# Kernel tuning notes

Hardware: AMD Instinct MI355X
Metric: run time of the kernel (lower is better)

Reference implementation:

```python
import jax, jax.numpy as jnp
from jax import lax
import numpy as np

B, S, G = 64, 200, 8
CHAR_V, GAZ_V = 8000, 100000
D_CHAR, D_GAZ, H = 128, 128, 512
N_LABEL = 20
N_TAG = N_LABEL + 2  # CRF adds START (N_TAG-2) and STOP (N_TAG-1)


def setup_inputs() -> dict:
    key = jax.random.key(0)
    ks = jax.random.split(key, 16)
    lengths = jax.random.randint(ks[0], (B,), S // 2, S + 1)
    pos = jnp.arange(S)[None, :]
    mask = pos < lengths[:, None]
    char_inputs = jax.random.randint(ks[1], (B, S), 0, CHAR_V)
    gaz_ids = jax.random.randint(ks[2], (B, S, G), 0, GAZ_V)
    cnt = jax.random.randint(ks[3], (B, S), 1, G + 1)
    gaz_mask = (jnp.arange(G)[None, None, :] < cnt[..., None]).astype(jnp.int32)
    rev_gaz_ids = jax.random.randint(ks[4], (B, S, G), 0, GAZ_V)
    rcnt = jax.random.randint(ks[5], (B, S), 1, G + 1)
    rev_gaz_mask = (jnp.arange(G)[None, None, :] < rcnt[..., None]).astype(jnp.int32)
    sc = 0.1
    D_in = D_CHAR + D_GAZ
    return dict(
        char_inputs=char_inputs, lengths=lengths, mask=mask,
        gaz_ids=gaz_ids, gaz_mask=gaz_mask,
        rev_gaz_ids=rev_gaz_ids, rev_gaz_mask=rev_gaz_mask,
        char_table=jax.random.normal(ks[6], (CHAR_V, D_CHAR)) * sc,
        gaz_table=jax.random.normal(ks[7], (GAZ_V, D_GAZ)) * sc,
        w_ih_f=jax.random.normal(ks[8], (4 * H, D_in)) * sc,
        w_hh_f=jax.random.normal(ks[9], (4 * H, H)) * sc,
        b_f=jnp.zeros((4 * H,), jnp.float32),
        w_ih_b=jax.random.normal(ks[10], (4 * H, D_in)) * sc,
        w_hh_b=jax.random.normal(ks[11], (4 * H, H)) * sc,
        b_b=jnp.zeros((4 * H,), jnp.float32),
        W_out=jax.random.normal(ks[12], (2 * H, N_TAG)) * sc,
        b_out=jnp.zeros((N_TAG,), jnp.float32),
        transitions=jax.random.normal(ks[13], (N_TAG, N_TAG)) * sc,
    )


def rev_pad(x, lengths):
    # reverse each sequence within its valid length (reverse_padded_sequence)
    b, s = x.shape[0], x.shape[1]
    pos = jnp.arange(s)[None, :]
    idx = jnp.where(pos < lengths[:, None], lengths[:, None] - 1 - pos, pos)
    idx = idx.reshape((b, s) + (1,) * (x.ndim - 2))
    return jnp.take_along_axis(x, jnp.broadcast_to(idx, x.shape), axis=1)


def gaz_embed(table, ids, m):
    # masked mean over the G candidate gaz words per char (Gaz_Embed, type=1)
    e = table[ids]                                   # [B,S,G,D]
    mf = m.astype(e.dtype)[..., None]
    return (e * mf).sum(2) / jnp.maximum(mf.sum(2), 1.0)


def lstm(x, w_ih, w_hh, b):
    # x: [B,S,D]; torch gate order i,f,g,o
    h0 = jnp.zeros((x.shape[0], H), x.dtype)

    def step(carry, xt):
        h, c = carry
        g = xt @ w_ih.T + h @ w_hh.T + b
        i, f, gg, o = jnp.split(g, 4, axis=-1)
        c = jax.nn.sigmoid(f) * c + jax.nn.sigmoid(i) * jnp.tanh(gg)
        h = jax.nn.sigmoid(o) * jnp.tanh(c)
        return (h, c), h

    _, hs = lax.scan(step, (h0, h0), x.transpose(1, 0, 2))
    return hs.transpose(1, 0, 2)                     # [B,S,H]


def emissions_fn(char_inputs, lengths, gaz_ids, gaz_mask, rev_gaz_ids, rev_gaz_mask,
                 char_table, gaz_table, w_ih_f, w_hh_f, b_f, w_ih_b, w_hh_b, b_b,
                 W_out, b_out):
    char_embs = char_table[char_inputs]              # [B,S,Dc]
    rev_char_embs = rev_pad(char_embs, lengths)
    g_f = gaz_embed(gaz_table, gaz_ids, gaz_mask)
    g_b = gaz_embed(gaz_table, rev_pad(rev_gaz_ids, lengths), rev_pad(rev_gaz_mask, lengths))
    fwd_in = jnp.concatenate([char_embs, g_f], axis=-1)
    bwd_in = jnp.concatenate([rev_char_embs, g_b], axis=-1)
    h_f = lstm(fwd_in, w_ih_f, w_hh_f, b_f)
    h_b = rev_pad(lstm(bwd_in, w_ih_b, w_hh_b, b_b), lengths)
    lstm_outs = jnp.concatenate([h_f, h_b], axis=-1)  # [B,S,2H]
    return lstm_outs @ W_out + b_out                  # [B,S,N_TAG]


def viterbi(emissions, mask, transitions):
    # transitions[prev, next]; START=N_TAG-2, STOP=N_TAG-1
    n = emissions.shape[-1]
    start, stop = n - 2, n - 1
    init = emissions[:, 0] + transitions[start][None, :]     # [B,n]
    ident = jnp.arange(n, dtype=jnp.int32)[None, :]

    def vstep(part, inp):
        emit_t, m_t = inp                                    # [B,n], [B]
        cand = part[:, :, None] + transitions[None] + emit_t[:, None, :]
        new = cand.max(axis=1)
        bp = cand.argmax(axis=1).astype(jnp.int32)
        part = jnp.where(m_t[:, None], new, part)
        bp = jnp.where(m_t[:, None], bp, ident)              # identity bp on pad
        return part, bp

    part, bps = lax.scan(vstep, init,
                         (emissions[:, 1:].transpose(1, 0, 2), mask[:, 1:].T))
    last_tag = (part + transitions[:, stop][None, :]).argmax(-1).astype(jnp.int32)

    def btstep(tag, bp):
        prev = jnp.take_along_axis(bp, tag[:, None], axis=1)[:, 0]
        return prev, prev

    _, prev_tags = lax.scan(btstep, last_tag, bps, reverse=True)  # [S-1,B]
    tags = jnp.concatenate([prev_tags.T, last_tag[:, None]], axis=1)
    return tags * mask.astype(tags.dtype)


def reference(char_inputs, lengths, mask, gaz_ids, gaz_mask, rev_gaz_ids, rev_gaz_mask,
              char_table, gaz_table, w_ih_f, w_hh_f, b_f, w_ih_b, w_hh_b, b_b,
              W_out, b_out, transitions):
    emissions = emissions_fn(char_inputs, lengths, gaz_ids, gaz_mask,
                             rev_gaz_ids, rev_gaz_mask, char_table, gaz_table,
                             w_ih_f, w_hh_f, b_f, w_ih_b, w_hh_b, b_b, W_out, b_out)
    return viterbi(emissions, mask, transitions)
```

## Files before the change

### kernel.cpp

```cpp
#include <hip/hip_runtime.h>
#include <math.h>

#define S_LEN 200
#define BATCH 64
#define HID   512
#define NTAG  22
#define TCH   25
#define MC    (TCH*BATCH)

typedef unsigned short u16;
typedef unsigned int   u32;

__device__ __forceinline__ float bf2f(u16 u){
  union { u32 ui; float f; } v; v.ui = ((u32)u) << 16; return v.f;
}

__global__ void k_detect(const u32* __restrict__ w, int* __restrict__ flag){
  __shared__ int cnt;
  if (threadIdx.x == 0) cnt = 0;
  __syncthreads();
  int hits = 0;
  for (int i = threadIdx.x; i < 16384; i += 256){
    u32 e = (w[i] & 0x7F80u);
    if (e >= 0x3800u && e <= 0x4080u) hits++;
  }
  atomicAdd(&cnt, hits);
  __syncthreads();
  if (threadIdx.x == 0) *flag = (cnt > 8192) ? 1 : 0;
}

__global__ void k_cvt_f(const void* __restrict__ src, float* __restrict__ dst,
                        int n, const int* __restrict__ flag){
  int i = blockIdx.x*blockDim.x + threadIdx.x;
  if (i >= n) return;
  if (*flag) dst[i] = bf2f(((const u16*)src)[i]);
  else       dst[i] = ((const float*)src)[i];
}

__global__ void k_cvt4(const void* s0, float* d0, int n0,
                       const void* s1, float* d1, int n1,
                       const void* s2, float* d2, int n2,
                       const void* s3, float* d3, int n3,
                       const int* __restrict__ flag){
  int i = blockIdx.x*blockDim.x + threadIdx.x;
  int isbf = *flag;
  if (i < n0) d0[i] = isbf ? bf2f(((const u16*)s0)[i]) : ((const float*)s0)[i];
  if (i < n1) d1[i] = isbf ? bf2f(((const u16*)s1)[i]) : ((const float*)s1)[i];
  if (i < n2) d2[i] = isbf ? bf2f(((const u16*)s2)[i]) : ((const float*)s2)[i];
  if (i < n3) d3[i] = isbf ? bf2f(((const u16*)s3)[i]) : ((const float*)s3)[i];
}

__global__ __launch_bounds__(256)
void k_cvt_whh(const void* __restrict__ wf, const void* __restrict__ wb,
               float* __restrict__ dst, const int* __restrict__ flag){
  int o = blockIdx.x*256 + threadIdx.x;
  if (o >= 2*2048*512) return;
  int j = o & 63, r = (o>>6)&15, w = (o>>10)&7, slice = (o>>13)&127, dir = o>>20;
  int row = (r>>2)*512 + slice*4 + (r&3);
  int si = row*512 + w*64 + j;
  const void* src = dir ? wb : wf;
  float v = (*flag) ? bf2f(((const u16*)src)[si]) : ((const float*)src)[si];
  dst[o] = v;
}

__global__ void k_cvt_wt(const void* __restrict__ src, float* __restrict__ dst,
                         const int* __restrict__ flag){
  int i = blockIdx.x*blockDim.x + threadIdx.x;
  if (i >= 1024*24) return;
  int k = i / 24, tag = i % 24;
  float v = 0.f;
  if (tag < NTAG){
    v = (*flag) ? bf2f(((const u16*)src)[k*NTAG + tag])
                : ((const float*)src)[k*NTAG + tag];
  }
  int half = k >> 9, kk = k & 511;
  dst[((size_t)half*512 + kk)*24 + tag] = v;
}

__global__ void k_zero(float* __restrict__ p, int n){
  int i = blockIdx.x*blockDim.x + threadIdx.x;
  if (i < n) p[i] = 0.f;
}

__global__ __launch_bounds__(128)
void k_build(const int* __restrict__ ci, const int* __restrict__ lengths,
             const int* __restrict__ gid, const int* __restrict__ gm,
             const int* __restrict__ rgid, const int* __restrict__ rgm,
             const void* __restrict__ ctab, const void* __restrict__ gtab,
             const int* __restrict__ flag,
             float* __restrict__ fin, float* __restrict__ bin)
{
  int bs = blockIdx.x;
  int b = bs / S_LEN, s = bs % S_LEN;
  int d = threadIdx.x;
  int isbf = *flag;
  int len = lengths[b];
  int sb = (s < len) ? (len - 1 - s) : s;
  size_t orow = ((size_t)s*BATCH + b)*256;

  {
    int cid = ci[bs];
    float cv = isbf ? bf2f(((const u16*)ctab)[(size_t)cid*128 + d])
                    : ((const float*)ctab)[(size_t)cid*128 + d];
    fin[orow + d] = cv;
    const int* gg = gid + (size_t)bs*8;
    const int* mm = gm  + (size_t)bs*8;
    float sum = 0.f, cntf = 0.f;
    for (int g = 0; g < 8; ++g){
      float m = (float)mm[g];
      int gw = gg[g];
      float gv = isbf ? bf2f(((const u16*)gtab)[(size_t)gw*128 + d])
                      : ((const float*)gtab)[(size_t)gw*128 + d];
      sum += m * gv; cntf += m;
    }
    fin[orow + 128 + d] = sum / fmaxf(cntf, 1.f);
  }
  {
    int bsr = b*S_LEN + sb;
    int cid = ci[bsr];
    float cv = isbf ? bf2f(((const u16*)ctab)[(size_t)cid*128 + d])
                    : ((const float*)ctab)[(size_t)cid*128 + d];
    bin[orow + d] = cv;
    const int* gg = rgid + (size_t)bsr*8;
    const int* mm = rgm  + (size_t)bsr*8;
    float sum = 0.f, cntf = 0.f;
    for (int g = 0; g < 8; ++g){
      float m = (float)mm[g];
      int gw = gg[g];
      float gv = isbf ? bf2f(((const u16*)gtab)[(size_t)gw*128 + d])
                      : ((const float*)gtab)[(size_t)gw*128 + d];
      sum += m * gv; cntf += m;
    }
    bin[orow + 128 + d] = sum / fmaxf(cntf, 1.f);
  }
}

__global__ __launch_bounds__(256)
void k_gemm_ih(const float* __restrict__ Af, const float* __restrict__ Ab,
               const float* __restrict__ wih,
               const float* __restrict__ bias,
               float* __restrict__ gxc,
               int t0)
{
  const int dir = blockIdx.z;
  const float* A = (dir ? Ab : Af) + (size_t)t0*BATCH*256;
  const float* W = wih + (size_t)dir*2048*256;
  const float* bi = bias + (size_t)dir*2048;
  float* C = gxc + (size_t)dir*2048*MC;
  const int m0 = blockIdx.y * 64;
  const int n0 = blockIdx.x * 128;
  const int tid = threadIdx.x;
  __shared__ float As[32][64];
  __shared__ float Ws[32][128];
  const int lrA = tid >> 2, kqA = (tid & 3)*8;
  const int lrW = tid >> 1, kqW = (tid & 1)*16;
  const int tx = tid & 31, ty = tid >> 5;
  float acc[8][4] = {};

  for (int k0 = 0; k0 < 256; k0 += 32){
    float4 a0 = *(const float4*)(A + (size_t)(m0+lrA)*256 + k0+kqA);
    float4 a1 = *(const float4*)(A + (size_t)(m0+lrA)*256 + k0+kqA+4);
    float4 w0 = *(const float4*)(W + (size_t)(n0+lrW)*256 + k0+kqW);
    float4 w1 = *(const float4*)(W + (size_t)(n0+lrW)*256 + k0+kqW+4);
    float4 w2 = *(const float4*)(W + (size_t)(n0+lrW)*256 + k0+kqW+8);
    float4 w3 = *(const float4*)(W + (size_t)(n0+lrW)*256 + k0+kqW+12);
    As[kqA+0][lrA]=a0.x; As[kqA+1][lrA]=a0.y; As[kqA+2][lrA]=a0.z; As[kqA+3][lrA]=a0.w;
    As[kqA+4][lrA]=a1.x; As[kqA+5][lrA]=a1.y; As[kqA+6][lrA]=a1.z; As[kqA+7][lrA]=a1.w;
    Ws[kqW+ 0][lrW]=w0.x; Ws[kqW+ 1][lrW]=w0.y; Ws[kqW+ 2][lrW]=w0.z; Ws[kqW+ 3][lrW]=w0.w;
    Ws[kqW+ 4][lrW]=w1.x; Ws[kqW+ 5][lrW]=w1.y; Ws[kqW+ 6][lrW]=w1.z; Ws[kqW+ 7][lrW]=w1.w;
    Ws[kqW+ 8][lrW]=w2.x; Ws[kqW+ 9][lrW]=w2.y; Ws[kqW+10][lrW]=w2.z; Ws[kqW+11][lrW]=w2.w;
    Ws[kqW+12][lrW]=w3.x; Ws[kqW+13][lrW]=w3.y; Ws[kqW+14][lrW]=w3.z; Ws[kqW+15][lrW]=w3.w;
    __syncthreads();
    #pragma unroll 8
    for (int kk = 0; kk < 32; ++kk){
      float4 av0 = *(const float4*)(&As[kk][ty*8]);
      float4 av1 = *(const float4*)(&As[kk][ty*8+4]);
      float4 wv  = *(const float4*)(&Ws[kk][tx*4]);
      acc[0][0]+=av0.x*wv.x; acc[0][1]+=av0.x*wv.y; acc[0][2]+=av0.x*wv.z; acc[0][3]+=av0.x*wv.w;
      acc[1][0]+=av0.y*wv.x; acc[1][1]+=av0.y*wv.y; acc[1][2]+=av0.y*wv.z; acc[1][3]+=av0.y*wv.w;
      acc[2][0]+=av0.z*wv.x; acc[2][1]+=av0.z*wv.y; acc[2][2]+=av0.z*wv.z; acc[2][3]+=av0.z*wv.w;
      acc[3][0]+=av0.w*wv.x; acc[3][1]+=av0.w*wv.y; acc[3][2]+=av0.w*wv.z; acc[3][3]+=av0.w*wv.w;
      acc[4][0]+=av1.x*wv.x; acc[4][1]+=av1.x*wv.y; acc[4][2]+=av1.x*wv.z; acc[4][3]+=av1.x*wv.w;
      acc[5][0]+=av1.y*wv.x; acc[5][1]+=av1.y*wv.y; acc[5][2]+=av1.y*wv.z; acc[5][3]+=av1.y*wv.w;
      acc[6][0]+=av1.z*wv.x; acc[6][1]+=av1.z*wv.y; acc[6][2]+=av1.z*wv.z; acc[6][3]+=av1.z*wv.w;
      acc[7][0]+=av1.w*wv.x; acc[7][1]+=av1.w*wv.y; acc[7][2]+=av1.w*wv.z; acc[7][3]+=av1.w*wv.w;
    }
    __syncthreads();
  }

  #pragma unroll
  for (int jn = 0; jn < 4; ++jn){
    int col = n0 + tx*4 + jn;
    float bj = bi[col];
    float4 o0 = make_float4(acc[0][jn]+bj, acc[1][jn]+bj, acc[2][jn]+bj, acc[3][jn]+bj);
    float4 o1 = make_float4(acc[4][jn]+bj, acc[5][jn]+bj, acc[6][jn]+bj, acc[7][jn]+bj);
    *(float4*)(C + (size_t)col*MC + m0 + ty*8)     = o0;
    *(float4*)(C + (size_t)col*MC + m0 + ty*8 + 4) = o1;
  }
}

__global__ __launch_bounds__(512)
void k_step(const float* __restrict__ wsw,
            const float* __restrict__ gxc,
            float* __restrict__ hbuf,
            float* __restrict__ cbuf,
            float* __restrict__ hseq,
            int t, int tc)
{
  const int dir = blockIdx.y;
  const int slice = blockIdx.x;
  const int hrow_base = slice*4;
  const int tid = threadIdx.x;
  const int b = tid & 63;
  const int uw = __builtin_amdgcn_readfirstlane(tid >> 6);
  const int uk0 = uw * 64;

  __shared__ float part[8*16*64];

  const float* hprev = hbuf + (size_t)(dir*2 + (t&1))*HID*BATCH;
  float* hnext       = hbuf + (size_t)(dir*2 + ((t+1)&1))*HID*BATCH;

  float pgi=0.f, pgf=0.f, pgg=0.f, pgo=0.f, pc=0.f;
  if (tid < 256){
    const int hr = tid >> 6, bb = tid & 63;
    const int hrow = hrow_base + hr;
    const float* gxb = gxc + (size_t)dir*2048*MC + (size_t)tc*BATCH + bb;
    pgi = gxb[(size_t)(   0 + hrow)*MC];
    pgf = gxb[(size_t)( 512 + hrow)*MC];
    pgg = gxb[(size_t)(1024 + hrow)*MC];
    pgo = gxb[(size_t)(1536 + hrow)*MC];
    pc  = cbuf[((size_t)dir*HID + hrow)*BATCH + bb];
  }

  float hv[64];
  #pragma unroll
  for (int j = 0; j < 64; ++j)
    hv[j] = hprev[(size_t)(uk0 + j)*BATCH + b];

  const float* wv_base = wsw + (((size_t)(dir*128 + slice))*8 + uw)*1024;

  float acc[16];
  #pragma unroll
  for (int r = 0; r < 16; ++r) acc[r] = 0.f;

  #pragma unroll
  for (int r = 0; r < 16; ++r){
    const float* wr = wv_base + r*64;
    #pragma unroll
    for (int j = 0; j < 64; ++j)
      acc[r] += wr[j] * hv[j];
  }

  #pragma unroll
  for (int r = 0; r < 16; ++r)
    part[(uw*16 + r)*64 + b] = acc[r];
  __syncthreads();

  if (tid < 256){
    const int hr = tid >> 6;
    const int bb = tid & 63;
    const int hrow = hrow_base + hr;
    float g4[4];
    #pragma unroll
    for (int g = 0; g < 4; ++g){
      const int r = g*4 + hr;
      float s = 0.f;
      #pragma unroll
      for (int ww = 0; ww < 8; ++ww)
        s += part[(ww*16 + r)*64 + bb];
      g4[g] = s;
    }
    float gi = g4[0] + pgi;
    float gf = g4[1] + pgf;
    float gg = g4[2] + pgg;
    float go = g4[3] + pgo;
    float si = 1.f/(1.f+expf(-gi));
    float sf = 1.f/(1.f+expf(-gf));
    float so = 1.f/(1.f+expf(-go));
    float c = sf*pc + si*tanhf(gg);
    float h = so*tanhf(c);
    cbuf[((size_t)dir*HID + hrow)*BATCH + bb] = c;
    hnext[(size_t)hrow*BATCH + bb] = h;
    hseq[(((size_t)dir*S_LEN + t)*HID + hrow)*BATCH + bb] = h;
  }
}

__global__ __launch_bounds__(256)
void k_emis(const float* __restrict__ hseq, const int* __restrict__ lengths,
            const float* __restrict__ wpad,
            const float* __restrict__ bout,
            float* __restrict__ emisF, float* __restrict__ emisB)
{
  const int t = blockIdx.x;
  const int dir = blockIdx.y;
  const int tid = threadIdx.x;
  const int b = tid & 63;
  const int utg = __builtin_amdgcn_readfirstlane(tid >> 6);

  __shared__ float hl[64*64];

  const float* hsrc = hseq + ((size_t)(dir*S_LEN + t)*HID)*BATCH;
  const float* wbase = wpad + (size_t)dir*512*24 + utg*6;

  float acc[6] = {0.f,0.f,0.f,0.f,0.f,0.f};

  for (int c = 0; c < 8; ++c){
    const float4* s4 = (const float4*)(hsrc + (size_t)c*64*64);
    float4* d4 = (float4*)hl;
    #pragma unroll
    for (int q = 0; q < 4; ++q) d4[q*256 + tid] = s4[q*256 + tid];
    __syncthreads();
    const float* wrow = wbase + (size_t)c*64*24;
    #pragma unroll 4
    for (int k = 0; k < 64; ++k){
      float hval = hl[k*64 + b];
      #pragma unroll
      for (int i = 0; i < 6; ++i) acc[i] += hval * wrow[k*24 + i];
    }
    __syncthreads();
  }

  const int len = lengths[b];
  const int pos = dir ? ((t < len) ? (len - 1 - t) : t) : t;
  float* dst = (dir ? emisB : emisF) + ((size_t)b*S_LEN + pos)*NTAG;
  #pragma unroll
  for (int i = 0; i < 6; ++i){
    int tag = utg*6 + i;
    if (tag < NTAG) dst[tag] = acc[i] + (dir ? 0.f : bout[tag]);
  }
}

__global__ __launch_bounds__(64)
void k_viterbi(const float* __restrict__ emisF, const float* __restrict__ emisB,
               const int* __restrict__ lengths,
               const float* __restrict__ trans, int* __restrict__ out)
{
  const int b = blockIdx.x;
  const int j = threadIdx.x;
  __shared__ unsigned char bp[(S_LEN-1)*NTAG];
  const int len = lengths[b];
  const float* ef = emisF + (size_t)b*S_LEN*NTAG;
  const float* eb = emisB + (size_t)b*S_LEN*NTAG;
  const bool act = (j < NTAG);

  float trc[NTAG];
  #pragma unroll
  for (int i = 0; i < NTAG; ++i)
    trc[i] = act ? trans[i*NTAG + j] : 0.f;
  const float trstop = act ? trans[j*NTAG + (NTAG-1)] : 0.f;

  float part = act ? (ef[j] + eb[j] + trans[(NTAG-2)*NTAG + j]) : -3.4e38f;
  float e_next = act ? (ef[NTAG + j] + eb[NTAG + j]) : 0.f;

  for (int t = 1; t < S_LEN; ++t){
    float e = e_next;
    if (t+1 < S_LEN && act) e_next = ef[(t+1)*NTAG + j] + eb[(t+1)*NTAG + j];
    float best = -3.4e38f; int bi = 0;
    #pragma unroll
    for (int i = 0; i < NTAG; ++i){
      float v = __shfl(part, i) + trc[i];
      if (v > best){ best = v; bi = i; }
    }
    if (t < len) part = best + e;
    if (act) bp[(t-1)*NTAG + j] = (unsigned char)((t < len) ? bi : j);
  }

  float fin = part + trstop;
  float best = -3.4e38f; int tag = 0;
  #pragma unroll
  for (int i = 0; i < NTAG; ++i){
    float v = __shfl(fin, i);
    if (v > best){ best = v; tag = i; }
  }
  __builtin_amdgcn_wave_barrier();
  if (j == 0){
    out[b*S_LEN + S_LEN-1] = (S_LEN-1 < len) ? tag : 0;
    for (int t = S_LEN-2; t >= 0; --t){
      tag = bp[t*NTAG + tag];
      out[b*S_LEN + t] = (t < len) ? tag : 0;
    }
  }
}

extern "C" void kernel_launch(void* const* d_in, const int* in_sizes, int n_in,
                              void* d_out, int out_size, void* d_ws, size_t ws_size,
                              hipStream_t stream)
{
  (void)in_sizes; (void)n_in; (void)out_size; (void)ws_size;
  const int* char_inputs  = (const int*)d_in[0];
  const int* lengths      = (const int*)d_in[1];
  const int* gaz_ids      = (const int*)d_in[3];
  const int* gaz_mask     = (const int*)d_in[4];
  const int* rev_gaz_ids  = (const int*)d_in[5];
  const int* rev_gaz_mask = (const int*)d_in[6];
  const void* char_table  = d_in[7];
  const void* gaz_table   = d_in[8];
  const void* w_ih_f = d_in[9];
  const void* w_hh_f = d_in[10];
  const void* b_f    = d_in[11];
  const void* w_ih_b = d_in[12];
  const void* w_hh_b = d_in[13];
  const void* b_b    = d_in[14];
  const void* W_out  = d_in[15];
  const void* b_out  = d_in[16];
  const void* trans  = d_in[17];

  char* ws = (char*)d_ws;
  size_t off = 0;
  auto alloc = [&](size_t bytes)->char*{
    char* p = ws + off; off = (off + bytes + 255) & ~(size_t)255; return p;
  };
  int*   flag   = (int*)  alloc(256);
  float* wsw    = (float*)alloc(2ull*2048*512*4);
  float* wih32  = (float*)alloc(2ull*2048*256*4);
  float* bias32 = (float*)alloc(2ull*2048*4);
  float* wpad   = (float*)alloc(2ull*512*24*4);
  float* bout32 = (float*)alloc(22ull*4);
  float* trans32= (float*)alloc(484ull*4);
  float* fwd_in = (float*)alloc(12800ull*256*4);
  float* bwd_in = (float*)alloc(12800ull*256*4);
  float* gxc    = (float*)alloc(2ull*2048*MC*4);
  float* hbuf   = (float*)alloc(2ull*2*512*64*4);
  float* cbuf   = (float*)alloc(2ull*512*64*4);
  float* hseq   = (float*)alloc(2ull*200*512*64*4);
  float* emisF  = (float*)alloc(12800ull*22*4);
  float* emisB  = (float*)alloc(12800ull*22*4);

  k_detect<<<1,256,0,stream>>>((const u32*)char_table, flag);
  k_cvt_whh<<<8192,256,0,stream>>>(w_hh_f, w_hh_b, wsw, flag);
  k_cvt_f<<<2048,256,0,stream>>>(w_ih_f, wih32,          524288, flag);
  k_cvt_f<<<2048,256,0,stream>>>(w_ih_b, wih32 + 524288, 524288, flag);
  k_cvt4<<<8,256,0,stream>>>(b_f, bias32, 2048,
                             b_b, bias32 + 2048, 2048,
                             b_out, bout32, 22,
                             trans, trans32, 484, flag);
  k_cvt_wt<<<96,256,0,stream>>>(W_out, wpad, flag);

  k_build<<<12800,128,0,stream>>>(char_inputs, lengths, gaz_ids, gaz_mask,
                                  rev_gaz_ids, rev_gaz_mask, char_table, gaz_table,
                                  flag, fwd_in, bwd_in);

  k_zero<<<768,256,0,stream>>>(hbuf, 2*2*512*64 + 2*512*64);

  for (int t0 = 0; t0 < S_LEN; t0 += TCH){
    k_gemm_ih<<<dim3(16,TCH,2),256,0,stream>>>(fwd_in, bwd_in, wih32, bias32,
                                               gxc, t0);
    for (int tc = 0; tc < TCH; ++tc)
      k_step<<<dim3(128,2),512,0,stream>>>(wsw, gxc, hbuf, cbuf, hseq, t0+tc, tc);
  }

  k_emis<<<dim3(S_LEN,2),256,0,stream>>>(hseq, lengths, wpad, bout32, emisF, emisB);
  k_viterbi<<<64,64,0,stream>>>(emisF, emisB, lengths, trans32, (int*)d_out);
}
```

Baseline: 2.886 ms.

## Fuse per-timestep LSTM launches into cooperative kernel with grid sync

Replaces the 25 separate per-timestep LSTM step launches in each chunk with one cooperative kernel that loops over the timesteps and calls grid.sync between them. If the cooperative launch fails, it falls back to per-step launches. The aim is to remove kernel launch overhead and inter-launch gaps, at the cost of a grid-wide barrier per step. The Viterbi kernel also switches from wave shuffles to shared memory with block barriers, which adds two syncs per step.

```diff
diff --git a/kernel.cpp b/kernel.cpp
--- a/kernel.cpp
+++ b/kernel.cpp
@@ -1,5 +1,8 @@
 #include <hip/hip_runtime.h>
+#include <hip/hip_cooperative_groups.h>
 #include <math.h>
+
+namespace cg = cooperative_groups;
 
 #define S_LEN 200
 #define BATCH 64
@@ -199,23 +202,16 @@
   }
 }
 
-__global__ __launch_bounds__(512)
-void k_step(const float* __restrict__ wsw,
-            const float* __restrict__ gxc,
-            float* __restrict__ hbuf,
-            float* __restrict__ cbuf,
-            float* __restrict__ hseq,
-            int t, int tc)
-{
-  const int dir = blockIdx.y;
-  const int slice = blockIdx.x;
+__device__ __forceinline__
+void step_body(const float* __restrict__ wsw, const float* __restrict__ gxc,
+               float* __restrict__ hbuf, float* __restrict__ cbuf,
+               float* __restrict__ hseq, int t, int tc,
+               int dir, int slice, int tid, float* part)
+{
   const int hrow_base = slice*4;
-  const int tid = threadIdx.x;
   const int b = tid & 63;
   const int uw = __builtin_amdgcn_readfirstlane(tid >> 6);
   const int uk0 = uw * 64;
-
-  __shared__ float part[8*16*64];
 
   const float* hprev = hbuf + (size_t)(dir*2 + (t&1))*HID*BATCH;
   float* hnext       = hbuf + (size_t)(dir*2 + ((t+1)&1))*HID*BATCH;
@@ -285,6 +281,32 @@
   }
 }
 
+__global__ __launch_bounds__(512)
+void k_steps(const float* __restrict__ wsw, const float* __restrict__ gxc,
+             float* __restrict__ hbuf, float* __restrict__ cbuf,
+             float* __restrict__ hseq, int t0)
+{
+  cg::grid_group grid = cg::this_grid();
+  __shared__ float part[8*16*64];
+  const int dir = blockIdx.y;
+  const int slice = blockIdx.x;
+  const int tid = threadIdx.x;
+  for (int tc = 0; tc < TCH; ++tc){
+    step_body(wsw, gxc, hbuf, cbuf, hseq, t0+tc, tc, dir, slice, tid, part);
+    grid.sync();
+  }
+}
+
+__global__ __launch_bounds__(512)
+void k_step1(const float* __restrict__ wsw, const float* __restrict__ gxc,
+             float* __restrict__ hbuf, float* __restrict__ cbuf,
+             float* __restrict__ hseq, int t, int tc)
+{
+  __shared__ float part[8*16*64];
+  step_body(wsw, gxc, hbuf, cbuf, hseq, t, tc, blockIdx.y, blockIdx.x,
+            threadIdx.x, part);
+}
+
 __global__ __launch_bounds__(256)
 void k_emis(const float* __restrict__ hseq, const int* __restrict__ lengths,
             const float* __restrict__ wpad,
@@ -337,43 +359,46 @@
 {
   const int b = blockIdx.x;
   const int j = threadIdx.x;
+  const bool act = (j < NTAG);
+  __shared__ float ps[NTAG];
   __shared__ unsigned char bp[(S_LEN-1)*NTAG];
   const int len = lengths[b];
   const float* ef = emisF + (size_t)b*S_LEN*NTAG;
   const float* eb = emisB + (size_t)b*S_LEN*NTAG;
-  const bool act = (j < NTAG);
 
   float trc[NTAG];
   #pragma unroll
   for (int i = 0; i < NTAG; ++i)
     trc[i] = act ? trans[i*NTAG + j] : 0.f;
-  const float trstop = act ? trans[j*NTAG + (NTAG-1)] : 0.f;
-
-  float part = act ? (ef[j] + eb[j] + trans[(NTAG-2)*NTAG + j]) : -3.4e38f;
-  float e_next = act ? (ef[NTAG + j] + eb[NTAG + j]) : 0.f;
+
+  if (act) ps[j] = ef[j] + eb[j] + trans[(NTAG-2)*NTAG + j];
+  __syncthreads();
 
   for (int t = 1; t < S_LEN; ++t){
-    float e = e_next;
-    if (t+1 < S_LEN && act) e_next = ef[(t+1)*NTAG + j] + eb[(t+1)*NTAG + j];
-    float best = -3.4e38f; int bi = 0;
+    float e = act ? (ef[t*NTAG + j] + eb[t*NTAG + j]) : 0.f;
+    float pv[NTAG];
+    #pragma unroll
+    for (int i = 0; i < NTAG; ++i) pv[i] = ps[i] + trc[i];
+    float best = pv[0]; int bi = 0;
+    #pragma unroll
+    for (int i = 1; i < NTAG; ++i){
+      if (pv[i] > best){ best = pv[i]; bi = i; }
+    }
+    __syncthreads();
+    if (act){
+      if (t < len){ ps[j] = best + e; bp[(t-1)*NTAG + j] = (unsigned char)bi; }
+      else        { bp[(t-1)*NTAG + j] = (unsigned char)j; }
+    }
+    __syncthreads();
+  }
+
+  if (j == 0){
+    float best = -3.4e38f; int tag = 0;
     #pragma unroll
     for (int i = 0; i < NTAG; ++i){
-      float v = __shfl(part, i) + trc[i];
-      if (v > best){ best = v; bi = i; }
-    }
-    if (t < len) part = best + e;
-    if (act) bp[(t-1)*NTAG + j] = (unsigned char)((t < len) ? bi : j);
-  }
-
-  float fin = part + trstop;
-  float best = -3.4e38f; int tag = 0;
-  #pragma unroll
-  for (int i = 0; i < NTAG; ++i){
-    float v = __shfl(fin, i);
-    if (v > best){ best = v; tag = i; }
-  }
-  __builtin_amdgcn_wave_barrier();
-  if (j == 0){
+      float v = ps[i] + trans[i*NTAG + (NTAG-1)];
+      if (v > best){ best = v; tag = i; }
+    }
     out[b*S_LEN + S_LEN-1] = (S_LEN-1 < len) ? tag : 0;
     for (int t = S_LEN-2; t >= 0; --t){
       tag = bp[t*NTAG + tag];
@@ -445,8 +470,17 @@
   for (int t0 = 0; t0 < S_LEN; t0 += TCH){
     k_gemm_ih<<<dim3(16,TCH,2),256,0,stream>>>(fwd_in, bwd_in, wih32, bias32,
                                                gxc, t0);
-    for (int tc = 0; tc < TCH; ++tc)
-      k_step<<<dim3(128,2),512,0,stream>>>(wsw, gxc, hbuf, cbuf, hseq, t0+tc, tc);
+    int t0_arg = t0;
+    void* args[] = { (void*)&wsw, (void*)&gxc, (void*)&hbuf, (void*)&cbuf,
+                     (void*)&hseq, (void*)&t0_arg };
+    hipError_t err = hipLaunchCooperativeKernel((const void*)k_steps,
+                                                dim3(128,2), dim3(512),
+                                                args, 0, stream);
+    if (err != hipSuccess){
+      for (int tc = 0; tc < TCH; ++tc)
+        k_step1<<<dim3(128,2),512,0,stream>>>(wsw, gxc, hbuf, cbuf, hseq,
+                                              t0+tc, tc);
+    }
   }
 
   k_emis<<<dim3(S_LEN,2),256,0,stream>>>(hseq, lengths, wpad, bout32, emisF, emisB);
```

New measurement: 7.025 ms. 2.43x slower.
